# Optimization experiments

Hardware: AMD Instinct MI355X
Metric: run time of the kernel (lower is better)

The kernel has to match this reference:

```python
import jax, jax.numpy as jnp
from jax import lax
import numpy as np

# Model dims (match init_kwargs / MolDecoder defaults)
V, E, H, Z, L, T = 64, 64, 256, 128, 3, 120
B = 4096


def _uinit(k, shape, fan):
    # PyTorch-style uniform(-1/sqrt(fan), 1/sqrt(fan)) init
    bound = 1.0 / np.sqrt(fan).astype(np.float32)
    return jax.random.uniform(k, shape, jnp.float32, -bound, bound)


def setup_inputs() -> dict:
    key = jax.random.key(0)
    ks = jax.random.split(key, 32)
    inp = {
        'z': jax.random.normal(ks[0], (B, Z), jnp.float32),
        # nn.Embedding with padding_idx=0 -> row 0 is zeros
        'emb': jax.random.normal(ks[1], (V, E), jnp.float32).at[0].set(0.0),
        'z2h_w': _uinit(ks[2], (H * L, Z), Z),
        'z2h_b': _uinit(ks[3], (H * L,), Z),
        'out_w': _uinit(ks[4], (V, H), H),
        'out_b': _uinit(ks[5], (V,), H),
    }
    kidx = 6
    for l in range(L):
        din = E if l == 0 else H
        inp[f'w_ih_{l}'] = _uinit(ks[kidx + 0], (3 * H, din), H)
        inp[f'w_hh_{l}'] = _uinit(ks[kidx + 1], (3 * H, H), H)
        inp[f'b_ih_{l}'] = _uinit(ks[kidx + 2], (3 * H,), H)
        inp[f'b_hh_{l}'] = _uinit(ks[kidx + 3], (3 * H,), H)
        kidx += 4
    return inp


def _gru_cell(x, h, wi, wh, bi, bh):
    # PyTorch GRUCell math
    gi = x @ wi.T + bi            # [B, 3H]
    gh = h @ wh.T + bh            # [B, 3H]
    ir, iz, inn = jnp.split(gi, 3, axis=-1)
    hr, hz, hn = jnp.split(gh, 3, axis=-1)
    r = jax.nn.sigmoid(ir + hr)
    u = jax.nn.sigmoid(iz + hz)
    n = jnp.tanh(inn + r * hn)
    return (1.0 - u) * n + u * h


def reference(z, emb, z2h_w, z2h_b, out_w, out_b,
              w_ih_0, w_hh_0, b_ih_0, b_hh_0,
              w_ih_1, w_hh_1, b_ih_1, b_hh_1,
              w_ih_2, w_hh_2, b_ih_2, b_hh_2):
    batch = z.shape[0]
    layers = [(w_ih_0, w_hh_0, b_ih_0, b_hh_0),
              (w_ih_1, w_hh_1, b_ih_1, b_hh_1),
              (w_ih_2, w_hh_2, b_ih_2, b_hh_2)]
    # z -> initial hidden [L, B, H]
    h0 = jnp.tanh(z @ z2h_w.T + z2h_b).reshape(batch, L, H).transpose(1, 0, 2)
    tok0 = jnp.ones((batch,), jnp.int32)  # start token = 1 (torch.ones)

    def step(carry, _):
        h, tok = carry
        x = emb[tok]                       # [B, E]
        new_h = []
        for l, (wi, wh, bi, bh) in enumerate(layers):
            hl = _gru_cell(x, h[l], wi, wh, bi, bh)
            new_h.append(hl)
            x = hl
        logits = x @ out_w.T + out_b       # [B, V]
        next_tok = jnp.argmax(logits, axis=-1).astype(jnp.int32)
        return (jnp.stack(new_h), next_tok), logits

    _, logits_seq = lax.scan(step, (h0, tok0), None, length=T - 1)
    return logits_seq.transpose(1, 0, 2)   # [B, T-1, V]
```

## Files before the change

kernel.cpp:

```cpp
#include <hip/hip_runtime.h>
#include <hip/hip_bf16.h>

typedef __bf16 bf16;
typedef __bf16 bf16x8 __attribute__((ext_vector_type(8)));
typedef float  f32x4  __attribute__((ext_vector_type(4)));

#define MFMA16(a,b,c) __builtin_amdgcn_mfma_f32_16x16x32_bf16((a),(b),(c),0,0,0)
#define NSTEP 119

#define O_L0   0u
#define O_L1   491520u
#define O_L2   1277952u
#define O_Z2H  2064384u
#define O_OUTW 2260992u
#define FXF   1146880u
#define FH0A  1409024u
#define FH0B  2457600u
#define FH1A  3506176u
#define FH1B  4554752u
#define FH2A  5603328u
#define FH2B  6651904u

#define FOFF(m,k) (((k)>>5)*512 + ((m) + 16*(((k)>>3)&3))*8 + ((k)&7))

__device__ __forceinline__ f32x4 splat4(float v){ f32x4 r={v,v,v,v}; return r; }
__device__ __forceinline__ float sigf(float x){ return 1.f/(1.f+expf(-x)); }

__global__ void pack2(const float* __restrict__ src, bf16* __restrict__ dst,
                      int Rt, int KTm, int KTg, int ktoff, int K) {
  int idx = blockIdx.x * 256 + threadIdx.x;
  if (idx >= Rt * KTm * 64) return;
  int lane = idx & 63, fi = idx >> 6;
  int r15 = lane & 15, q = lane >> 4;
  int c = fi / KTm, ktm = fi - c * KTm;
  const float* s = src + (size_t)(c * 16 + r15) * K + ktm * 32 + q * 8;
  bf16* d = dst + (size_t)(c * KTg + ktoff + ktm) * 1024 + lane * 8;
  #pragma unroll
  for (int e = 0; e < 8; ++e) {
    float v = s[e];
    bf16 hi = (bf16)v;
    d[e] = hi;
    d[e + 512] = (bf16)(v - (float)hi);
  }
}

__global__ __launch_bounds__(512)
void kinit(const float* __restrict__ z, const float* __restrict__ emb,
           const float* __restrict__ z2h_b, const bf16* __restrict__ wsb,
           float* __restrict__ xf, float* __restrict__ h0,
           float* __restrict__ h1, float* __restrict__ h2)
{
  __shared__ __align__(16) bf16 zF[2][2048];
  const int tid = threadIdx.x, wv = tid >> 6, lane = tid & 63;
  const int q = lane >> 4, r15 = lane & 15;
  const int rt = blockIdx.x, b0 = rt * 16;
  {
    const int m = tid >> 5, c4 = (tid & 31) * 4;
    float4 v = *(const float4*)(z + (size_t)(b0 + m) * 128 + c4);
    const float vv[4] = {v.x, v.y, v.z, v.w};
    #pragma unroll
    for (int e = 0; e < 4; ++e) {
      int off = FOFF(m, c4 + e);
      bf16 hi = (bf16)vv[e];
      zF[0][off] = hi;
      zF[1][off] = (bf16)(vv[e] - (float)hi);
    }
  }
  for (int i = tid; i < 1024; i += 512) {
    int m = i >> 6, e = i & 63;
    xf[(size_t)rt * 1024 + FOFF(m, e)] = emb[64 + e];
  }
  __syncthreads();
  f32x4 acc[6];
  #pragma unroll
  for (int t = 0; t < 6; ++t) acc[t] = splat4(z2h_b[(wv * 6 + t) * 16 + r15]);
  #pragma unroll
  for (int kt = 0; kt < 4; ++kt) {
    bf16x8 a0 = *(const bf16x8*)(&zF[0][kt * 512 + lane * 8]);
    bf16x8 a1 = *(const bf16x8*)(&zF[1][kt * 512 + lane * 8]);
    #pragma unroll
    for (int t = 0; t < 6; ++t) {
      const bf16* bb = wsb + O_Z2H + (size_t)((wv * 6 + t) * 4 + kt) * 1024 + lane * 8;
      bf16x8 b0 = *(const bf16x8*)bb;
      bf16x8 b1 = *(const bf16x8*)(bb + 512);
      acc[t] = MFMA16(a0, b0, acc[t]);
      acc[t] = MFMA16(a1, b0, acc[t]);
      acc[t] = MFMA16(a0, b1, acc[t]);
    }
  }
  #pragma unroll
  for (int t = 0; t < 6; ++t) {
    const int col = (wv * 6 + t) * 16 + r15;
    const int lay = col >> 8, j = col & 255;
    float* H = lay == 0 ? h0 : lay == 1 ? h1 : h2;
    #pragma unroll
    for (int r = 0; r < 4; ++r)
      H[(size_t)rt * 4096 + FOFF(q * 4 + r, j)] = tanhf(acc[t][r]);
  }
}

template<int L>
__global__ __launch_bounds__(512)
void kgate(const float* __restrict__ ain, const float* __restrict__ hin,
           float* __restrict__ hout,
           const float* __restrict__ bih, const float* __restrict__ bhh,
           const bf16* __restrict__ wsb)
{
  constexpr int KTI = (L == 0) ? 2 : 8;
  constexpr int KT  = KTI + 8;
  constexpr int PH  = (L == 0) ? 10 : 8;
  constexpr int NPH = (L == 0) ? 1 : 2;
  constexpr int AST = (L == 0) ? 1024 : 4096;
  const size_t WB = (L == 0) ? O_L0 : (L == 1) ? O_L1 : O_L2;

  __shared__ __align__(16) bf16 WS[PH][6][1024];

  const int tid = threadIdx.x, wv = tid >> 6, lane = tid & 63;
  const int q = lane >> 4, r15 = lane & 15;
  const int rg = blockIdx.x >> 3, cg = blockIdx.x & 7;
  const int rt = rg * 8 + wv;

  const float* Ain = ain + (size_t)rt * AST;
  const float* Ah  = hin + (size_t)rt * 4096;

  f32x4 accR[2], accZ[2], accNI[2], accNH[2];
  #pragma unroll
  for (int c = 0; c < 2; ++c) {
    accR[c] = splat4(0.f); accZ[c] = splat4(0.f);
    accNI[c] = splat4(0.f); accNH[c] = splat4(0.f);
  }

  #pragma unroll
  for (int p = 0; p < NPH; ++p) {
    const int kb = p * PH;
    for (int u = wv; u < 6 * PH; u += 8) {
      int ct = u % 6, ktp = u / 6;
      int c = (ct >> 1) * 16 + cg * 2 + (ct & 1);
      const bf16* src = wsb + WB + (size_t)(c * KT + kb + ktp) * 1024 + lane * 8;
      bf16x8 t0 = *(const bf16x8*)src;
      bf16x8 t1 = *(const bf16x8*)(src + 512);
      *(bf16x8*)(&WS[ktp][ct][lane * 8]) = t0;
      *(bf16x8*)(&WS[ktp][ct][512 + lane * 8]) = t1;
    }
    __syncthreads();
    const float* ap0 = (kb < KTI) ? (Ain + (size_t)kb * 512 + lane * 8)
                                  : (Ah + (size_t)(kb - KTI) * 512 + lane * 8);
    float4 va = *(const float4*)ap0;
    float4 vb = *(const float4*)(ap0 + 4);
    #pragma unroll
    for (int ktp = 0; ktp < PH; ++ktp) {
      const int kt = kb + ktp;
      float4 na, nb;
      if (ktp + 1 < PH) {
        const int kn = kt + 1;
        const float* apn = (kn < KTI) ? (Ain + (size_t)kn * 512 + lane * 8)
                                      : (Ah + (size_t)(kn - KTI) * 512 + lane * 8);
        na = *(const float4*)apn;
        nb = *(const float4*)(apn + 4);
      }
      const float vv[8] = {va.x, va.y, va.z, va.w, vb.x, vb.y, vb.z, vb.w};
      bf16x8 a0, a1;
      #pragma unroll
      for (int e = 0; e < 8; ++e) {
        bf16 hi = (bf16)vv[e];
        a0[e] = hi;
        a1[e] = (bf16)(vv[e] - (float)hi);
      }
      #pragma unroll
      for (int ct = 0; ct < 6; ++ct) {
        bf16x8 b0 = *(const bf16x8*)(&WS[ktp][ct][lane * 8]);
        bf16x8 b1 = *(const bf16x8*)(&WS[ktp][ct][512 + lane * 8]);
        f32x4* acc;
        const int ctl = ct & 1;
        if (ct < 2)      acc = &accR[ctl];
        else if (ct < 4) acc = &accZ[ctl];
        else             acc = (kt < KTI) ? &accNI[ctl] : &accNH[ctl];
        *acc = MFMA16(a0, b0, *acc);
        *acc = MFMA16(a1, b0, *acc);
        *acc = MFMA16(a0, b1, *acc);
      }
      va = na; vb = nb;
    }
    if (p + 1 < NPH) __syncthreads();
  }

  #pragma unroll
  for (int ctl = 0; ctl < 2; ++ctl) {
    const int j = cg * 32 + ctl * 16 + r15;
    const float brz = bih[j] + bhh[j];
    const float bz  = bih[256 + j] + bhh[256 + j];
    const float bni = bih[512 + j];
    const float bnh = bhh[512 + j];
    #pragma unroll
    for (int r = 0; r < 4; ++r) {
      const int m = q * 4 + r;
      const size_t idx = (size_t)rt * 4096 + FOFF(m, j);
      float rg_ = sigf(accR[ctl][r] + brz);
      float zg  = sigf(accZ[ctl][r] + bz);
      float ng  = tanhf(accNI[ctl][r] + bni + rg_ * (accNH[ctl][r] + bnh));
      float hp  = hin[idx];
      hout[idx] = (1.f - zg) * ng + zg * hp;
    }
  }
}

__global__ __launch_bounds__(512)
void klogits(const float* __restrict__ h2, float* __restrict__ xf,
             const float* __restrict__ emb, const float* __restrict__ out_b,
             const bf16* __restrict__ wsb, float* __restrict__ out, int step)
{
  __shared__ float logS2[2][16][68];
  const int tid = threadIdx.x, wv = tid >> 6, lane = tid & 63;
  const int q = lane >> 4, r15 = lane & 15;
  const int rt = blockIdx.x;
  const float* A = h2 + (size_t)rt * 4096;

  {
    const int ks = wv >> 2, tt = wv & 3;
    f32x4 acc = ks ? splat4(0.f) : splat4(out_b[tt * 16 + r15]);
    #pragma unroll
    for (int kt2 = 0; kt2 < 4; ++kt2) {
      const int kg = ks * 4 + kt2;
      float4 v0 = *(const float4*)(A + kg * 512 + lane * 8);
      float4 v1 = *(const float4*)(A + kg * 512 + lane * 8 + 4);
      const float vv[8] = {v0.x, v0.y, v0.z, v0.w, v1.x, v1.y, v1.z, v1.w};
      bf16x8 a0, a1;
      #pragma unroll
      for (int e = 0; e < 8; ++e) {
        bf16 hi = (bf16)vv[e];
        a0[e] = hi;
        a1[e] = (bf16)(vv[e] - (float)hi);
      }
      const bf16* bb = wsb + O_OUTW + (size_t)(tt * 8 + kg) * 1024 + lane * 8;
      bf16x8 b0 = *(const bf16x8*)bb;
      bf16x8 b1 = *(const bf16x8*)(bb + 512);
      acc = MFMA16(a0, b0, acc);
      acc = MFMA16(a1, b0, acc);
      acc = MFMA16(a0, b1, acc);
    }
    #pragma unroll
    for (int r = 0; r < 4; ++r)
      logS2[ks][q * 4 + r][tt * 16 + r15] = acc[r];
  }
  __syncthreads();
  #pragma unroll
  for (int k2 = 0; k2 < 2; ++k2) {
    const int rr = wv * 2 + k2;
    float v = logS2[0][rr][lane] + logS2[1][rr][lane];
    out[((size_t)(rt * 16 + rr) * NSTEP + step) * 64 + lane] = v;
    float bv = v; int bi = lane;
    #pragma unroll
    for (int d = 1; d < 64; d <<= 1) {
      float ov = __shfl_xor(bv, d);
      int   oi = __shfl_xor(bi, d);
      if (ov > bv || (ov == bv && oi < bi)) { bv = ov; bi = oi; }
    }
    xf[(size_t)rt * 1024 + FOFF(rr, lane)] = emb[(size_t)bi * 64 + lane];
  }
}

extern "C" void kernel_launch(void* const* d_in, const int* in_sizes, int n_in,
                              void* d_out, int out_size, void* d_ws, size_t ws_size,
                              hipStream_t stream) {
  bf16*  wsb = (bf16*)d_ws;
  float* wsf = (float*)d_ws;
  const float* z     = (const float*)d_in[0];
  const float* emb   = (const float*)d_in[1];
  const float* z2h_b = (const float*)d_in[3];
  const float* out_b = (const float*)d_in[5];
  const float* bih0 = (const float*)d_in[8],  *bhh0 = (const float*)d_in[9];
  const float* bih1 = (const float*)d_in[12], *bhh1 = (const float*)d_in[13];
  const float* bih2 = (const float*)d_in[16], *bhh2 = (const float*)d_in[17];
  float* out = (float*)d_out;

  float* xf    = wsf + FXF;
  float* h0[2] = {wsf + FH0A, wsf + FH0B};
  float* h1[2] = {wsf + FH1A, wsf + FH1B};
  float* h2[2] = {wsf + FH2A, wsf + FH2B};

  pack2<<<24, 256, 0, stream>>>((const float*)d_in[6],  wsb + O_L0,  48, 2, 10, 0, 64);
  pack2<<<96, 256, 0, stream>>>((const float*)d_in[7],  wsb + O_L0,  48, 8, 10, 2, 256);
  pack2<<<96, 256, 0, stream>>>((const float*)d_in[10], wsb + O_L1,  48, 8, 16, 0, 256);
  pack2<<<96, 256, 0, stream>>>((const float*)d_in[11], wsb + O_L1,  48, 8, 16, 8, 256);
  pack2<<<96, 256, 0, stream>>>((const float*)d_in[14], wsb + O_L2,  48, 8, 16, 0, 256);
  pack2<<<96, 256, 0, stream>>>((const float*)d_in[15], wsb + O_L2,  48, 8, 16, 8, 256);
  pack2<<<48, 256, 0, stream>>>((const float*)d_in[2],  wsb + O_Z2H, 48, 4, 4,  0, 128);
  pack2<<<8,  256, 0, stream>>>((const float*)d_in[4],  wsb + O_OUTW, 4, 8, 8,  0, 256);

  kinit<<<256, 512, 0, stream>>>(z, emb, z2h_b, wsb, xf, h0[0], h1[0], h2[0]);

  for (int t = 0; t < NSTEP; ++t) {
    const int p = t & 1, pn = p ^ 1;
    kgate<0><<<256, 512, 0, stream>>>(xf,     h0[p], h0[pn], bih0, bhh0, wsb);
    kgate<1><<<256, 512, 0, stream>>>(h0[pn], h1[p], h1[pn], bih1, bhh1, wsb);
    kgate<2><<<256, 512, 0, stream>>>(h1[pn], h2[p], h2[pn], bih2, bhh2, wsb);
    klogits<<<256, 512, 0, stream>>>(h2[pn], xf, emb, out_b, wsb, out, t);
  }
}
```

Measured before the change: 6.596 ms.

## Fuse all timesteps into one persistent cooperative kernel with grid syncs

Replaces the roughly 476 per-step kernel launches (three GRU layers plus logits for each of 119 steps) with a single cooperative kernel of 256 blocks. Each phase is separated by a grid-wide sync, and shared memory is one union buffer reused across phases. The goal is to remove per-launch overhead and the gaps between kernels. In exchange it adds about 476 grid barriers, limits the kernel to one block per CU, and needs the whole grid to be co-resident. The weight tiles are still reloaded from global memory every phase.

Result: slower. 20.10 ms (+204.7%).

```diff
diff --git a/kernel.cpp b/kernel.cpp
--- a/kernel.cpp
+++ b/kernel.cpp
@@ -1,5 +1,8 @@
 #include <hip/hip_runtime.h>
 #include <hip/hip_bf16.h>
+#include <hip/hip_cooperative_groups.h>
+
+namespace cg = cooperative_groups;
 
 typedef __bf16 bf16;
 typedef __bf16 bf16x8 __attribute__((ext_vector_type(8)));
@@ -15,11 +18,9 @@
 #define O_OUTW 2260992u
 #define FXF   1146880u
 #define FH0A  1409024u
-#define FH0B  2457600u
 #define FH1A  3506176u
-#define FH1B  4554752u
 #define FH2A  5603328u
-#define FH2B  6651904u
+#define HPAR  1048576u
 
 #define FOFF(m,k) (((k)>>5)*512 + ((m) + 16*(((k)>>3)&3))*8 + ((k)&7))
 
@@ -44,13 +45,15 @@
   }
 }
 
-__global__ __launch_bounds__(512)
-void kinit(const float* __restrict__ z, const float* __restrict__ emb,
-           const float* __restrict__ z2h_b, const bf16* __restrict__ wsb,
-           float* __restrict__ xf, float* __restrict__ h0,
-           float* __restrict__ h1, float* __restrict__ h2)
+
+__device__ void init_phase(const float* __restrict__ z, const float* __restrict__ emb,
+                           const float* __restrict__ z2h_b, const bf16* __restrict__ wsb,
+                           float* __restrict__ xf, float* __restrict__ h0,
+                           float* __restrict__ h1, float* __restrict__ h2,
+                           bf16* __restrict__ WSf)
 {
-  __shared__ __align__(16) bf16 zF[2][2048];
+  bf16* zF0 = WSf;
+  bf16* zF1 = WSf + 2048;
   const int tid = threadIdx.x, wv = tid >> 6, lane = tid & 63;
   const int q = lane >> 4, r15 = lane & 15;
   const int rt = blockIdx.x, b0 = rt * 16;
@@ -62,8 +65,8 @@
     for (int e = 0; e < 4; ++e) {
       int off = FOFF(m, c4 + e);
       bf16 hi = (bf16)vv[e];
-      zF[0][off] = hi;
-      zF[1][off] = (bf16)(vv[e] - (float)hi);
+      zF0[off] = hi;
+      zF1[off] = (bf16)(vv[e] - (float)hi);
     }
   }
   for (int i = tid; i < 1024; i += 512) {
@@ -76,8 +79,8 @@
   for (int t = 0; t < 6; ++t) acc[t] = splat4(z2h_b[(wv * 6 + t) * 16 + r15]);
   #pragma unroll
   for (int kt = 0; kt < 4; ++kt) {
-    bf16x8 a0 = *(const bf16x8*)(&zF[0][kt * 512 + lane * 8]);
-    bf16x8 a1 = *(const bf16x8*)(&zF[1][kt * 512 + lane * 8]);
+    bf16x8 a0 = *(const bf16x8*)(zF0 + kt * 512 + lane * 8);
+    bf16x8 a1 = *(const bf16x8*)(zF1 + kt * 512 + lane * 8);
     #pragma unroll
     for (int t = 0; t < 6; ++t) {
       const bf16* bb = wsb + O_Z2H + (size_t)((wv * 6 + t) * 4 + kt) * 1024 + lane * 8;
@@ -100,11 +103,10 @@
 }
 
 template<int L>
-__global__ __launch_bounds__(512)
-void kgate(const float* __restrict__ ain, const float* __restrict__ hin,
-           float* __restrict__ hout,
-           const float* __restrict__ bih, const float* __restrict__ bhh,
-           const bf16* __restrict__ wsb)
+__device__ void gate_phase(const float* __restrict__ ain, const float* __restrict__ hin,
+                           float* __restrict__ hout,
+                           const float* __restrict__ bih, const float* __restrict__ bhh,
+                           const bf16* __restrict__ wsb, bf16* __restrict__ WSf)
 {
   constexpr int KTI = (L == 0) ? 2 : 8;
   constexpr int KT  = KTI + 8;
@@ -112,8 +114,6 @@
   constexpr int NPH = (L == 0) ? 1 : 2;
   constexpr int AST = (L == 0) ? 1024 : 4096;
   const size_t WB = (L == 0) ? O_L0 : (L == 1) ? O_L1 : O_L2;
-
-  __shared__ __align__(16) bf16 WS[PH][6][1024];
 
   const int tid = threadIdx.x, wv = tid >> 6, lane = tid & 63;
   const int q = lane >> 4, r15 = lane & 15;
@@ -139,8 +139,8 @@
       const bf16* src = wsb + WB + (size_t)(c * KT + kb + ktp) * 1024 + lane * 8;
       bf16x8 t0 = *(const bf16x8*)src;
       bf16x8 t1 = *(const bf16x8*)(src + 512);
-      *(bf16x8*)(&WS[ktp][ct][lane * 8]) = t0;
-      *(bf16x8*)(&WS[ktp][ct][512 + lane * 8]) = t1;
+      *(bf16x8*)(WSf + (ktp * 6 + ct) * 1024 + lane * 8) = t0;
+      *(bf16x8*)(WSf + (ktp * 6 + ct) * 1024 + 512 + lane * 8) = t1;
     }
     __syncthreads();
     const float* ap0 = (kb < KTI) ? (Ain + (size_t)kb * 512 + lane * 8)
@@ -168,8 +168,8 @@
       }
       #pragma unroll
       for (int ct = 0; ct < 6; ++ct) {
-        bf16x8 b0 = *(const bf16x8*)(&WS[ktp][ct][lane * 8]);
-        bf16x8 b1 = *(const bf16x8*)(&WS[ktp][ct][512 + lane * 8]);
+        bf16x8 b0 = *(const bf16x8*)(WSf + (ktp * 6 + ct) * 1024 + lane * 8);
+        bf16x8 b1 = *(const bf16x8*)(WSf + (ktp * 6 + ct) * 1024 + 512 + lane * 8);
         f32x4* acc;
         const int ctl = ct & 1;
         if (ct < 2)      acc = &accR[ctl];
@@ -204,12 +204,11 @@
   }
 }
 
-__global__ __launch_bounds__(512)
-void klogits(const float* __restrict__ h2, float* __restrict__ xf,
-             const float* __restrict__ emb, const float* __restrict__ out_b,
-             const bf16* __restrict__ wsb, float* __restrict__ out, int step)
+__device__ void logits_phase(const float* __restrict__ h2, float* __restrict__ xf,
+                             const float* __restrict__ emb, const float* __restrict__ out_b,
+                             const bf16* __restrict__ wsb, float* __restrict__ out,
+                             int step, float (*logS2)[16][68])
 {
-  __shared__ float logS2[2][16][68];
   const int tid = threadIdx.x, wv = tid >> 6, lane = tid & 63;
   const int q = lane >> 4, r15 = lane & 15;
   const int rt = blockIdx.x;
@@ -257,6 +256,43 @@
     }
     xf[(size_t)rt * 1024 + FOFF(rr, lane)] = emb[(size_t)bi * 64 + lane];
   }
+  __syncthreads();
+}
+
+__global__ __launch_bounds__(512, 1)
+void moldec_coop(const float* __restrict__ z, const float* __restrict__ emb,
+                 const float* __restrict__ z2h_b, const float* __restrict__ out_b,
+                 const float* __restrict__ bih0, const float* __restrict__ bhh0,
+                 const float* __restrict__ bih1, const float* __restrict__ bhh1,
+                 const float* __restrict__ bih2, const float* __restrict__ bhh2,
+                 const bf16* __restrict__ wsb, float* __restrict__ wsf,
+                 float* __restrict__ out)
+{
+  __shared__ __align__(16) bf16 WSf[10 * 6 * 1024];
+  __shared__ float logS2[2][16][68];
+  cg::grid_group gg = cg::this_grid();
+
+  float* xf = wsf + FXF;
+
+  init_phase(z, emb, z2h_b, wsb, xf,
+             wsf + FH0A, wsf + FH1A, wsf + FH2A, WSf);
+  gg.sync();
+
+  for (int t = 0; t < NSTEP; ++t) {
+    const size_t p = (size_t)(t & 1) * HPAR, pn = (size_t)((t & 1) ^ 1) * HPAR;
+    float* h0i = wsf + FH0A + p;  float* h0o = wsf + FH0A + pn;
+    float* h1i = wsf + FH1A + p;  float* h1o = wsf + FH1A + pn;
+    float* h2i = wsf + FH2A + p;  float* h2o = wsf + FH2A + pn;
+
+    gate_phase<0>(xf,  h0i, h0o, bih0, bhh0, wsb, WSf);
+    gg.sync();
+    gate_phase<1>(h0o, h1i, h1o, bih1, bhh1, wsb, WSf);
+    gg.sync();
+    gate_phase<2>(h1o, h2i, h2o, bih2, bhh2, wsb, WSf);
+    gg.sync();
+    logits_phase(h2o, xf, emb, out_b, wsb, out, t, logS2);
+    gg.sync();
+  }
 }
 
 extern "C" void kernel_launch(void* const* d_in, const int* in_sizes, int n_in,
@@ -273,11 +309,6 @@
   const float* bih2 = (const float*)d_in[16], *bhh2 = (const float*)d_in[17];
   float* out = (float*)d_out;
 
-  float* xf    = wsf + FXF;
-  float* h0[2] = {wsf + FH0A, wsf + FH0B};
-  float* h1[2] = {wsf + FH1A, wsf + FH1B};
-  float* h2[2] = {wsf + FH2A, wsf + FH2B};
-
   pack2<<<24, 256, 0, stream>>>((const float*)d_in[6],  wsb + O_L0,  48, 2, 10, 0, 64);
   pack2<<<96, 256, 0, stream>>>((const float*)d_in[7],  wsb + O_L0,  48, 8, 10, 2, 256);
   pack2<<<96, 256, 0, stream>>>((const float*)d_in[10], wsb + O_L1,  48, 8, 16, 0, 256);
@@ -287,13 +318,10 @@
   pack2<<<48, 256, 0, stream>>>((const float*)d_in[2],  wsb + O_Z2H, 48, 4, 4,  0, 128);
   pack2<<<8,  256, 0, stream>>>((const float*)d_in[4],  wsb + O_OUTW, 4, 8, 8,  0, 256);
 
-  kinit<<<256, 512, 0, stream>>>(z, emb, z2h_b, wsb, xf, h0[0], h1[0], h2[0]);
-
-  for (int t = 0; t < NSTEP; ++t) {
-    const int p = t & 1, pn = p ^ 1;
-    kgate<0><<<256, 512, 0, stream>>>(xf,     h0[p], h0[pn], bih0, bhh0, wsb);
-    kgate<1><<<256, 512, 0, stream>>>(h0[pn], h1[p], h1[pn], bih1, bhh1, wsb);
-    kgate<2><<<256, 512, 0, stream>>>(h1[pn], h2[p], h2[pn], bih2, bhh2, wsb);
-    klogits<<<256, 512, 0, stream>>>(h2[pn], xf, emb, out_b, wsb, out, t);
-  }
-}
+  void* args[] = {(void*)&z, (void*)&emb, (void*)&z2h_b, (void*)&out_b,
+                  (void*)&bih0, (void*)&bhh0, (void*)&bih1, (void*)&bhh1,
+                  (void*)&bih2, (void*)&bhh2,
+                  (void*)&wsb, (void*)&wsf, (void*)&out};
+  hipLaunchCooperativeKernel((void*)moldec_coop, dim3(256), dim3(512),
+                             args, 0, stream);
+}
```
